# Performance work log

Hardware: AMD Instinct MI355X
Metric: run time of the kernel (lower is better)

The kernel has to match this reference:

```python
import math
import jax, jax.numpy as jnp
import numpy as np

D_MODEL = 1024
N_HEADS = 16
HEAD_DIM = D_MODEL // N_HEADS
ROPE_BASE = 10000.0
EPS = 1e-6


def rmsnorm(x, w, eps=EPS):
    # x: (..., head_dim); computed in fp32 like the torch code
    xf = x.astype(jnp.float32)
    rms = jax.lax.rsqrt(jnp.mean(xf * xf, axis=-1, keepdims=True) + eps)
    return (xf * rms).astype(x.dtype) * w


def apply_rope(x, cos, sin):
    # x: (B, H, T, head_dim); cos/sin: (T, head_dim/2)
    d2 = x.shape[-1] // 2
    x1, x2 = x[..., :d2], x[..., d2:]
    c = cos[None, None, :, :]
    s = sin[None, None, :, :]
    return jnp.concatenate([x1 * c - x2 * s, x2 * c + x1 * s], axis=-1)


def setup_inputs() -> dict:
    key = jax.random.key(0)
    ks = jax.random.split(key, 7)
    B, T = 2, 2048
    x = jax.random.normal(ks[0], (B, T, D_MODEL), dtype=jnp.float32)
    scale = 1.0 / math.sqrt(D_MODEL)
    Wq = jax.random.normal(ks[1], (D_MODEL, D_MODEL), dtype=jnp.float32) * scale
    Wk = jax.random.normal(ks[2], (D_MODEL, D_MODEL), dtype=jnp.float32) * scale
    Wv = jax.random.normal(ks[3], (D_MODEL, D_MODEL), dtype=jnp.float32) * scale
    Wo = jax.random.normal(ks[4], (D_MODEL, D_MODEL), dtype=jnp.float32) * scale
    q_norm_w = jnp.ones((HEAD_DIM,), dtype=jnp.float32)
    k_norm_w = jnp.ones((HEAD_DIM,), dtype=jnp.float32)
    return {"x": x, "Wq": Wq, "Wk": Wk, "Wv": Wv, "Wo": Wo,
            "q_norm_w": q_norm_w, "k_norm_w": k_norm_w}


def reference(x, Wq, Wk, Wv, Wo, q_norm_w, k_norm_w):
    B, T, d = x.shape
    H, hd = N_HEADS, HEAD_DIM
    # projections (nn.Linear applies x @ W.T; here W is stored as (in,out))
    q = (x @ Wq).reshape(B, T, H, hd).transpose(0, 2, 1, 3)  # (B,H,T,hd)
    k = (x @ Wk).reshape(B, T, H, hd).transpose(0, 2, 1, 3)
    v = (x @ Wv).reshape(B, T, H, hd).transpose(0, 2, 1, 3)
    # QK RMSNorm per head
    q = rmsnorm(q, q_norm_w)
    k = rmsnorm(k, k_norm_w)
    # rotary embeddings
    inv_freq = 1.0 / (ROPE_BASE ** (jnp.arange(0, hd, 2, dtype=jnp.float32) / hd))
    t = jnp.arange(T, dtype=jnp.float32)
    freqs = jnp.outer(t, inv_freq)  # (T, hd/2)
    cos, sin = jnp.cos(freqs), jnp.sin(freqs)
    q = apply_rope(q, cos, sin)
    k = apply_rope(k, cos, sin)
    # naive full attention with causal mask
    scale = 1.0 / math.sqrt(hd)
    attn = jnp.einsum('bhqd,bhkd->bhqk', q, k) * scale  # (B,H,T,T)
    causal = jnp.triu(jnp.full((T, T), -jnp.inf, dtype=attn.dtype), k=1)
    attn = attn + causal[None, None, :, :]
    attn = jax.nn.softmax(attn, axis=-1)
    out = jnp.einsum('bhqk,bhkd->bhqd', attn, v)
    out = out.transpose(0, 2, 1, 3).reshape(B, T, d)
    return out @ Wo
```

## Files before the change

### kernel.cpp

```cpp
#include <hip/hip_runtime.h>

typedef unsigned short u16;
typedef unsigned int   u32;
typedef __bf16 bf16x8 __attribute__((ext_vector_type(8)));
typedef float  f32x4  __attribute__((ext_vector_type(4)));
typedef float  f32x2  __attribute__((ext_vector_type(2)));
typedef u32    u32x4  __attribute__((ext_vector_type(4)));
typedef u16    u16x4  __attribute__((ext_vector_type(4)));

#define D_MODEL 1024
#define T_SEQ   2048
#define NH      16
#define HD      64

#define QSCALE  0.18033688011112042f
#define NEG8L2E -11.541560327111707f

__device__ __forceinline__ float b2f(u16 u){ return __uint_as_float(((u32)u)<<16); }
__device__ __forceinline__ u16 f2b(float f){
  u32 x = __float_as_uint(f);
  x += 0x7fffu + ((x>>16)&1u);
  return (u16)(x>>16);
}

__device__ __forceinline__ void gll16(const void* g, void* l){
  __builtin_amdgcn_global_load_lds((const __attribute__((address_space(1))) unsigned int*)g,
                                   (__attribute__((address_space(3))) unsigned int*)l, 16, 0, 0);
}

__global__ __launch_bounds__(256) void prep(
    const float* __restrict__ X, u16* __restrict__ Xb,
    const float* __restrict__ W0, const float* __restrict__ W1,
    const float* __restrict__ W2, const float* __restrict__ W3,
    u16* __restrict__ T0, u16* __restrict__ T1,
    u16* __restrict__ T2, u16* __restrict__ T3,
    float* __restrict__ cs)
{
  __shared__ u16 s[32][33];
  const int id = blockIdx.x, tid = threadIdx.x;
  if (id < 4096){
    const int i = (id*256 + tid)<<2;
    f32x4 v = *(const f32x4*)(X + i);
    u16x4 o;
    o[0]=f2b(v[0]); o[1]=f2b(v[1]); o[2]=f2b(v[2]); o[3]=f2b(v[3]);
    *(u16x4*)(Xb + i) = o;
  } else if (id < 8192){
    const int wid = id - 4096;
    const int z = wid >> 10, tile = wid & 1023;
    const float* src = (z==0)?W0:(z==1)?W1:(z==2)?W2:W3;
    u16*         dst = (z==0)?T0:(z==1)?T1:(z==2)?T2:T3;
    const int x = tid & 31, y = tid >> 5;
    const int r0 = (tile>>5)*32, c0 = (tile&31)*32;
    #pragma unroll
    for (int r=0;r<4;r++) s[y + r*8][x] = f2b(src[(r0 + y + r*8)*D_MODEL + c0 + x]);
    __syncthreads();
    #pragma unroll
    for (int r=0;r<4;r++) dst[(c0 + y + r*8)*D_MODEL + r0 + x] = s[x][y + r*8];
  } else {
    const int gid = (id-8192)*256 + tid;
    const int t = gid >> 5, fi = gid & 31;
    const float invf = expf(-(float)fi * 0.2878231366242558f);
    float sn, cn;
    sincosf((float)t * invf, &sn, &cn);
    cs[gid*2]   = cn;
    cs[gid*2+1] = sn;
  }
}

__global__ __launch_bounds__(256) void gemm_qkv(
    const u16* __restrict__ A, const u16* __restrict__ Bt,
    const float* __restrict__ qw, const float* __restrict__ kw,
    const float* __restrict__ cs,
    u16* __restrict__ Qb, u16* __restrict__ Kb, u16* __restrict__ Vt)
{
  __shared__ __align__(16) u16 sA[1024*8];
  __shared__ __align__(16) u16 sB[1024*8];
  const int id = blockIdx.x;
  const int xcd = id & 7, slot = id >> 3;
  const int bn = (xcd & 1)*12 + (slot % 12);
  const int bm = (xcd >> 1)*8 + (slot / 12);
  const int bm0 = bm<<7, bn0 = bn<<7;

  const int tid = threadIdx.x;
  const int lane = tid & 63;
  const int w  = tid>>6;
  const int wm = (w>>1)<<6;
  const int wn = (w&1)<<6;
  const int quad = lane>>4, lr = lane&15;
  const int swl = lr & 7;

  int rS[4], cS[4];
  #pragma unroll
  for (int i=0;i<4;i++){
    int s = i*256 + tid;
    rS[i] = s>>3;
    cS[i] = (s&7) ^ (rS[i]&7);
  }

  const f32x4 z4 = {0.f,0.f,0.f,0.f};
  f32x4 acc[4][4];
  #pragma unroll
  for (int i=0;i<4;i++)
    #pragma unroll
    for (int j=0;j<4;j++) acc[i][j] = z4;

  for (int kt=0; kt<D_MODEL; kt+=64){
    #pragma unroll
    for (int i=0;i<4;i++)
      gll16(A  + (bm0+rS[i])*D_MODEL + kt + cS[i]*8, sA + (i*256 + w*64)*8);
    #pragma unroll
    for (int i=0;i<4;i++)
      gll16(Bt + (bn0+rS[i])*D_MODEL + kt + cS[i]*8, sB + (i*256 + w*64)*8);
    __syncthreads();
    #pragma unroll
    for (int kk=0; kk<2; ++kk){
      bf16x8 af[4], bfr[4];
      const int cq = (kk*4 + quad) ^ swl;
      #pragma unroll
      for (int i=0;i<4;i++) af[i]  = *(const bf16x8*)(sA + ((wm + (i<<4) + lr)*8 + cq)*8);
      #pragma unroll
      for (int j=0;j<4;j++) bfr[j] = *(const bf16x8*)(sB + ((wn + (j<<4) + lr)*8 + cq)*8);
      #pragma unroll
      for (int i=0;i<4;i++)
        #pragma unroll
        for (int j=0;j<4;j++)
          acc[i][j] = __builtin_amdgcn_mfma_f32_16x16x32_bf16(af[i], bfr[j], acc[i][j], 0, 0, 0);
    }
    __syncthreads();
  }

  const int z = bn0 >> 10;
  const int ncl = bn0 & 1023;
  const int rq = quad<<2;

  if (z == 2){
    #pragma unroll
    for (int i=0;i<4;i++){
      int row0 = bm0 + wm + (i<<4) + rq;
      int bb = row0 >> 11, tt = row0 & (T_SEQ-1);
      #pragma unroll
      for (int j=0;j<4;j++){
        int nv = ncl + wn + (j<<4) + lr;
        int hh = nv >> 6, dd = nv & 63;
        u16* basep = Vt + ((bb*NH + hh)*HD + dd)*T_SEQ;
        #pragma unroll
        for (int r=0;r<4;r++){
          int t = tt + r;
          int pt = (t & ~63) + ((t&15)<<2) + ((t>>4)&3);
          basep[pt] = f2b(acc[i][j][r]);
        }
      }
    }
  } else {
    const float* w_ = (z==0) ? qw : kw;
    u16* dst = (z==0) ? Qb : Kb;
    const float scale = (z==0) ? QSCALE : 1.0f;
    float wv[4];
    #pragma unroll
    for (int j=0;j<4;j++) wv[j] = w_[(j<<4) + lr];
    #pragma unroll
    for (int i=0;i<4;i++){
      #pragma unroll
      for (int r=0;r<4;r++){
        const int grow = bm0 + wm + (i<<4) + rq + r;
        float ss = 0.f;
        #pragma unroll
        for (int j=0;j<4;j++) ss += acc[i][j][r]*acc[i][j][r];
        #pragma unroll
        for (int off=8; off>=1; off>>=1) ss += __shfl_xor(ss, off, 64);
        const float rms = rsqrtf(ss*(1.0f/64.0f) + 1e-6f);
        float xn[4];
        #pragma unroll
        for (int j=0;j<4;j++) xn[j] = acc[i][j][r]*rms*wv[j];
        const int t = grow & (T_SEQ-1);
        f32x2 c0 = *(const f32x2*)(cs + (t*32 + lr)*2);
        f32x2 c1 = *(const f32x2*)(cs + (t*32 + 16 + lr)*2);
        float o0 = xn[0]*c0[0] - xn[2]*c0[1];
        float o2 = xn[2]*c0[0] + xn[0]*c0[1];
        float o1 = xn[1]*c1[0] - xn[3]*c1[1];
        float o3 = xn[3]*c1[0] + xn[1]*c1[1];
        u16* rp = dst + grow*D_MODEL + ncl + wn + lr;
        rp[0]  = f2b(o0*scale);
        rp[16] = f2b(o1*scale);
        rp[32] = f2b(o2*scale);
        rp[48] = f2b(o3*scale);
      }
    }
  }
}

__global__ __launch_bounds__(256) void gemm_out(
    const u16* __restrict__ A, const u16* __restrict__ Bt, float* __restrict__ out)
{
  __shared__ __align__(16) u16 sA[512*8];
  __shared__ __align__(16) u16 sB[1024*8];
  const int id = blockIdx.x;
  const int xcd = id & 7, slot = id >> 3;
  const int bm = xcd*8 + (slot>>3);
  const int bn = slot & 7;
  const int bm0 = bm<<6, bn0 = bn<<7;

  const int tid = threadIdx.x;
  const int lane = tid & 63;
  const int w  = tid>>6;
  const int wm = (w>>1)<<5;
  const int wn = (w&1)<<6;
  const int quad = lane>>4, lr = lane&15;
  const int swl = lr & 7;

  int rS[4], cS[4];
  #pragma unroll
  for (int i=0;i<4;i++){
    int s = i*256 + tid;
    rS[i] = s>>3;
    cS[i] = (s&7) ^ (rS[i]&7);
  }

  const f32x4 z4 = {0.f,0.f,0.f,0.f};
  f32x4 acc[2][4];
  #pragma unroll
  for (int i=0;i<2;i++)
    #pragma unroll
    for (int j=0;j<4;j++) acc[i][j] = z4;

  for (int kt=0; kt<D_MODEL; kt+=64){
    #pragma unroll
    for (int i=0;i<2;i++)
      gll16(A  + (bm0+rS[i])*D_MODEL + kt + cS[i]*8, sA + (i*256 + w*64)*8);
    #pragma unroll
    for (int i=0;i<4;i++)
      gll16(Bt + (bn0+rS[i])*D_MODEL + kt + cS[i]*8, sB + (i*256 + w*64)*8);
    __syncthreads();
    #pragma unroll
    for (int kk=0; kk<2; ++kk){
      bf16x8 af[2], bfr[4];
      const int cq = (kk*4 + quad) ^ swl;
      #pragma unroll
      for (int i=0;i<2;i++) af[i]  = *(const bf16x8*)(sA + ((wm + (i<<4) + lr)*8 + cq)*8);
      #pragma unroll
      for (int j=0;j<4;j++) bfr[j] = *(const bf16x8*)(sB + ((wn + (j<<4) + lr)*8 + cq)*8);
      #pragma unroll
      for (int i=0;i<2;i++)
        #pragma unroll
        for (int j=0;j<4;j++)
          acc[i][j] = __builtin_amdgcn_mfma_f32_16x16x32_bf16(af[i], bfr[j], acc[i][j], 0, 0, 0);
    }
    __syncthreads();
  }

  const int rq = quad<<2;
  #pragma unroll
  for (int i=0;i<2;i++){
    #pragma unroll
    for (int r=0;r<4;r++){
      const int grow = bm0 + wm + (i<<4) + rq + r;
      #pragma unroll
      for (int j=0;j<4;j++)
        out[grow*D_MODEL + bn0 + wn + (j<<4) + lr] = acc[i][j][r];
    }
  }
}

__global__ __launch_bounds__(256) void attn_mfma(const u16* __restrict__ Qb, const u16* __restrict__ Kb,
                                                 const u16* __restrict__ Vt, u16* __restrict__ AO)
{
  __shared__ __align__(16) u16 sK [2][4096];
  __shared__ __align__(16) u16 sVT[2][4096];
  __shared__ __align__(16) u16 sP [4][1024];
  const int tid = threadIdx.x;
  const int h  = blockIdx.x, b = blockIdx.y;
  const int qt = 31 - blockIdx.z;
  const int w = tid>>6, lane = tid&63;
  const int quad = lane>>4, lr = lane&15;
  const int q8 = quad<<3;

  const int s0 = w*64 + lane, s1 = 256 + w*64 + lane;
  const int r0s = s0>>3, c0s = (s0&7)^(r0s&7);
  const int r1s = s1>>3, c1s = (s1&7)^(r1s&7);
  const u16* Kbase = Kb + (b*T_SEQ)*D_MODEL + h*HD;
  const u16* Vbase = Vt + (b*NH + h)*HD*T_SEQ;
  const int ldsOff0 = (w*64)*8, ldsOff1 = (256 + w*64)*8;

  const u16* Qrow = Qb + (b*T_SEQ + qt*64 + w*16 + lr)*D_MODEL + h*HD;
  bf16x8 qf0 = *(const bf16x8*)(Qrow + q8);
  bf16x8 qf1 = *(const bf16x8*)(Qrow + 32 + q8);

  f32x4 o[4];
  float lp[4];
  const f32x4 z4 = {0.f,0.f,0.f,0.f};
  const f32x4 ci = {NEG8L2E, NEG8L2E, NEG8L2E, NEG8L2E};
  #pragma unroll
  for (int r=0;r<4;r++) lp[r] = 0.f;
  #pragma unroll
  for (int nt=0;nt<4;nt++) o[nt] = z4;

  u16* myP = sP[w];

  gll16(Kbase + r0s*D_MODEL + c0s*8, &sK[0][ldsOff0]);
  gll16(Kbase + r1s*D_MODEL + c1s*8, &sK[0][ldsOff1]);
  gll16(Vbase + r0s*T_SEQ + c0s*8,   &sVT[0][ldsOff0]);
  gll16(Vbase + r1s*T_SEQ + c1s*8,   &sVT[0][ldsOff1]);
  __syncthreads();

  for (int kt=0; kt<=qt; ++kt){
    const int cur = kt&1;
    if (kt < qt){
      const int kn = kt+1, nb = cur^1;
      gll16(Kbase + (kn*64 + r0s)*D_MODEL + c0s*8, &sK[nb][ldsOff0]);
      gll16(Kbase + (kn*64 + r1s)*D_MODEL + c1s*8, &sK[nb][ldsOff1]);
      gll16(Vbase + r0s*T_SEQ + kn*64 + c0s*8,     &sVT[nb][ldsOff0]);
      gll16(Vbase + r1s*T_SEQ + kn*64 + c1s*8,     &sVT[nb][ldsOff1]);
    }

    f32x4 s4[4];
    #pragma unroll
    for (int ct=0; ct<4; ++ct){
      const int row = ct*16 + lr;
      const int sw = row&7;
      bf16x8 k0 = *(const bf16x8*)(&sK[cur][(row*8 + (quad     ^ sw))*8]);
      bf16x8 k1 = *(const bf16x8*)(&sK[cur][(row*8 + ((4+quad) ^ sw))*8]);
      f32x4 acc = ci;
      acc = __builtin_amdgcn_mfma_f32_16x16x32_bf16(qf0, k0, acc, 0,0,0);
      acc = __builtin_amdgcn_mfma_f32_16x16x32_bf16(qf1, k1, acc, 0,0,0);
      s4[ct] = acc;
    }

    if (kt == qt){
      #pragma unroll
      for (int ct=0; ct<4; ++ct){
        int col = ct*16 + lr;
        #pragma unroll
        for (int r=0;r<4;r++)
          if (col > w*16 + quad*4 + r) s4[ct][r] = -1e30f;
      }
    }

    #pragma unroll
    for (int r=0;r<4;r++){
      u16x4 pk;
      #pragma unroll
      for (int ct=0; ct<4; ++ct){
        float p = exp2f(s4[ct][r]);
        u32 pu = __float_as_uint(p) & 0xffff0000u;
        lp[r] += __uint_as_float(pu);
        pk[ct] = (u16)(pu>>16);
      }
      const int prow = quad*4 + r;
      const int pidx = prow*64 + (((lr>>1) ^ (prow&7))<<3) + ((lr&1)<<2);
      *(u16x4*)(myP + pidx) = pk;
    }

    #pragma unroll
    for (int st=0; st<2; ++st){
      bf16x8 pf = *(const bf16x8*)(myP + lr*64 + (((st*4+quad) ^ (lr&7))<<3));
      #pragma unroll
      for (int nt=0;nt<4;nt++){
        const int row = nt*16 + lr;
        const int slotv = row*8 + ((st*4+quad) ^ (row&7));
        bf16x8 vf = *(const bf16x8*)(&sVT[cur][slotv*8]);
        o[nt] = __builtin_amdgcn_mfma_f32_16x16x32_bf16(pf, vf, o[nt], 0,0,0);
      }
    }
    __syncthreads();
  }

  #pragma unroll
  for (int r=0;r<4;r++){
    #pragma unroll
    for (int off=8; off>=1; off>>=1) lp[r] += __shfl_xor(lp[r], off, 64);
  }
  const int rowg = b*T_SEQ + qt*64 + w*16 + quad*4;
  #pragma unroll
  for (int r=0;r<4;r++){
    float inv = 1.0f / lp[r];
    #pragma unroll
    for (int nt=0;nt<4;nt++)
      AO[(rowg + r)*D_MODEL + h*HD + nt*16 + lr] = f2b(o[nt][r]*inv);
  }
}

extern "C" void kernel_launch(void* const* d_in, const int* in_sizes, int n_in,
                              void* d_out, int out_size, void* d_ws, size_t ws_size,
                              hipStream_t stream)
{
  const float* X  = (const float*)d_in[0];
  const float* Wq = (const float*)d_in[1];
  const float* Wk = (const float*)d_in[2];
  const float* Wv = (const float*)d_in[3];
  const float* Wo = (const float*)d_in[4];
  const float* qw = (const float*)d_in[5];
  const float* kw = (const float*)d_in[6];

  char* ws = (char*)d_ws;
  const size_t MB = 1024*1024;
  u16*   WqkvT = (u16*)(ws + 0*MB);
  u16*   WoT   = (u16*)(ws + 6*MB);
  u16*   Xb    = (u16*)(ws + 8*MB);
  u16*   Qb    = (u16*)(ws + 16*MB);
  u16*   Kb    = (u16*)(ws + 24*MB);
  u16*   Vt    = (u16*)(ws + 32*MB);
  u16*   AO    = (u16*)(ws + 40*MB);
  float* CS    = (float*)(ws + 48*MB);

  prep<<<dim3(8448), 256, 0, stream>>>(X, Xb, Wq, Wk, Wv, Wo,
      WqkvT, WqkvT + 1024*1024, WqkvT + 2*1024*1024, WoT, CS);
  gemm_qkv<<<dim3(768), 256, 0, stream>>>(Xb, WqkvT, qw, kw, CS, Qb, Kb, Vt);
  attn_mfma<<<dim3(NH, 2, 32), 256, 0, stream>>>(Qb, Kb, Vt, AO);
  gemm_out<<<dim3(512), 256, 0, stream>>>(AO, WoT, (float*)d_out);
}
```

Before: 185.9 us.

## Vectorize weight transpose, halve gemm_out M-tile, single-buffer V in attention

The weight transpose in prep now reads float4 and writes u16x4 per thread instead of scalar accesses, to cut memory instructions. gemm_out switches to 32-row tiles with twice as many blocks, aiming for better occupancy and CU coverage at the cost of more B-tile reloads. The attention kernel drops V double buffering: it loads V into one LDS buffer at the start of each iteration and adds a barrier before the PV matmul. This saves LDS but puts the V load latency on the critical path, and the extra barrier adds synchronization cost.

```diff
diff --git a/kernel.cpp b/kernel.cpp
--- a/kernel.cpp
+++ b/kernel.cpp
@@ -49,13 +49,16 @@
     const int z = wid >> 10, tile = wid & 1023;
     const float* src = (z==0)?W0:(z==1)?W1:(z==2)?W2:W3;
     u16*         dst = (z==0)?T0:(z==1)?T1:(z==2)?T2:T3;
-    const int x = tid & 31, y = tid >> 5;
+    const int x = tid & 7, y = tid >> 3;
     const int r0 = (tile>>5)*32, c0 = (tile&31)*32;
-    #pragma unroll
-    for (int r=0;r<4;r++) s[y + r*8][x] = f2b(src[(r0 + y + r*8)*D_MODEL + c0 + x]);
-    __syncthreads();
-    #pragma unroll
-    for (int r=0;r<4;r++) dst[(c0 + y + r*8)*D_MODEL + r0 + x] = s[x][y + r*8];
+    f32x4 v = *(const f32x4*)(src + (r0 + y)*D_MODEL + c0 + 4*x);
+    #pragma unroll
+    for (int k=0;k<4;k++) s[y][4*x+k] = f2b(v[k]);
+    __syncthreads();
+    u16x4 o;
+    #pragma unroll
+    for (int k=0;k<4;k++) o[k] = s[4*x+k][y];
+    *(u16x4*)(dst + (c0 + y)*D_MODEL + r0 + 4*x) = o;
   } else {
     const int gid = (id-8192)*256 + tid;
     const int t = gid >> 5, fi = gid & 31;
@@ -192,72 +195,62 @@
 __global__ __launch_bounds__(256) void gemm_out(
     const u16* __restrict__ A, const u16* __restrict__ Bt, float* __restrict__ out)
 {
-  __shared__ __align__(16) u16 sA[512*8];
+  __shared__ __align__(16) u16 sA[256*8];
   __shared__ __align__(16) u16 sB[1024*8];
   const int id = blockIdx.x;
   const int xcd = id & 7, slot = id >> 3;
-  const int bm = xcd*8 + (slot>>3);
+  const int bm = xcd*16 + (slot>>3);
   const int bn = slot & 7;
-  const int bm0 = bm<<6, bn0 = bn<<7;
+  const int bm0 = bm<<5, bn0 = bn<<7;
 
   const int tid = threadIdx.x;
   const int lane = tid & 63;
   const int w  = tid>>6;
-  const int wm = (w>>1)<<5;
+  const int wm = (w>>1)<<4;
   const int wn = (w&1)<<6;
   const int quad = lane>>4, lr = lane&15;
   const int swl = lr & 7;
 
-  int rS[4], cS[4];
+  const int rA = tid>>3, cA = (tid&7) ^ (rA&7);
+  int rB[4], cB[4];
   #pragma unroll
   for (int i=0;i<4;i++){
     int s = i*256 + tid;
-    rS[i] = s>>3;
-    cS[i] = (s&7) ^ (rS[i]&7);
+    rB[i] = s>>3;
+    cB[i] = (s&7) ^ (rB[i]&7);
   }
 
   const f32x4 z4 = {0.f,0.f,0.f,0.f};
-  f32x4 acc[2][4];
-  #pragma unroll
-  for (int i=0;i<2;i++)
-    #pragma unroll
-    for (int j=0;j<4;j++) acc[i][j] = z4;
+  f32x4 acc[4];
+  #pragma unroll
+  for (int j=0;j<4;j++) acc[j] = z4;
 
   for (int kt=0; kt<D_MODEL; kt+=64){
-    #pragma unroll
-    for (int i=0;i<2;i++)
-      gll16(A  + (bm0+rS[i])*D_MODEL + kt + cS[i]*8, sA + (i*256 + w*64)*8);
+    gll16(A + (bm0+rA)*D_MODEL + kt + cA*8, sA + (w*64)*8);
     #pragma unroll
     for (int i=0;i<4;i++)
-      gll16(Bt + (bn0+rS[i])*D_MODEL + kt + cS[i]*8, sB + (i*256 + w*64)*8);
+      gll16(Bt + (bn0+rB[i])*D_MODEL + kt + cB[i]*8, sB + (i*256 + w*64)*8);
     __syncthreads();
     #pragma unroll
     for (int kk=0; kk<2; ++kk){
-      bf16x8 af[2], bfr[4];
       const int cq = (kk*4 + quad) ^ swl;
-      #pragma unroll
-      for (int i=0;i<2;i++) af[i]  = *(const bf16x8*)(sA + ((wm + (i<<4) + lr)*8 + cq)*8);
-      #pragma unroll
-      for (int j=0;j<4;j++) bfr[j] = *(const bf16x8*)(sB + ((wn + (j<<4) + lr)*8 + cq)*8);
-      #pragma unroll
-      for (int i=0;i<2;i++)
-        #pragma unroll
-        for (int j=0;j<4;j++)
-          acc[i][j] = __builtin_amdgcn_mfma_f32_16x16x32_bf16(af[i], bfr[j], acc[i][j], 0, 0, 0);
+      bf16x8 af = *(const bf16x8*)(sA + ((wm + lr)*8 + cq)*8);
+      #pragma unroll
+      for (int j=0;j<4;j++){
+        bf16x8 bfr = *(const bf16x8*)(sB + ((wn + (j<<4) + lr)*8 + cq)*8);
+        acc[j] = __builtin_amdgcn_mfma_f32_16x16x32_bf16(af, bfr, acc[j], 0, 0, 0);
+      }
     }
     __syncthreads();
   }
 
   const int rq = quad<<2;
   #pragma unroll
-  for (int i=0;i<2;i++){
-    #pragma unroll
-    for (int r=0;r<4;r++){
-      const int grow = bm0 + wm + (i<<4) + rq + r;
-      #pragma unroll
-      for (int j=0;j<4;j++)
-        out[grow*D_MODEL + bn0 + wn + (j<<4) + lr] = acc[i][j][r];
-    }
+  for (int r=0;r<4;r++){
+    const int grow = bm0 + wm + rq + r;
+    #pragma unroll
+    for (int j=0;j<4;j++)
+      out[grow*D_MODEL + bn0 + wn + (j<<4) + lr] = acc[j][r];
   }
 }
 
@@ -265,7 +258,7 @@
                                                  const u16* __restrict__ Vt, u16* __restrict__ AO)
 {
   __shared__ __align__(16) u16 sK [2][4096];
-  __shared__ __align__(16) u16 sVT[2][4096];
+  __shared__ __align__(16) u16 sV [4096];
   __shared__ __align__(16) u16 sP [4][1024];
   const int tid = threadIdx.x;
   const int h  = blockIdx.x, b = blockIdx.y;
@@ -298,8 +291,6 @@
 
   gll16(Kbase + r0s*D_MODEL + c0s*8, &sK[0][ldsOff0]);
   gll16(Kbase + r1s*D_MODEL + c1s*8, &sK[0][ldsOff1]);
-  gll16(Vbase + r0s*T_SEQ + c0s*8,   &sVT[0][ldsOff0]);
-  gll16(Vbase + r1s*T_SEQ + c1s*8,   &sVT[0][ldsOff1]);
   __syncthreads();
 
   for (int kt=0; kt<=qt; ++kt){
@@ -308,9 +299,9 @@
       const int kn = kt+1, nb = cur^1;
       gll16(Kbase + (kn*64 + r0s)*D_MODEL + c0s*8, &sK[nb][ldsOff0]);
       gll16(Kbase + (kn*64 + r1s)*D_MODEL + c1s*8, &sK[nb][ldsOff1]);
-      gll16(Vbase + r0s*T_SEQ + kn*64 + c0s*8,     &sVT[nb][ldsOff0]);
-      gll16(Vbase + r1s*T_SEQ + kn*64 + c1s*8,     &sVT[nb][ldsOff1]);
-    }
+    }
+    gll16(Vbase + r0s*T_SEQ + kt*64 + c0s*8, &sV[ldsOff0]);
+    gll16(Vbase + r1s*T_SEQ + kt*64 + c1s*8, &sV[ldsOff1]);
 
     f32x4 s4[4];
     #pragma unroll
@@ -350,6 +341,8 @@
       *(u16x4*)(myP + pidx) = pk;
     }
 
+    __syncthreads();
+
     #pragma unroll
     for (int st=0; st<2; ++st){
       bf16x8 pf = *(const bf16x8*)(myP + lr*64 + (((st*4+quad) ^ (lr&7))<<3));
@@ -357,7 +350,7 @@
       for (int nt=0;nt<4;nt++){
         const int row = nt*16 + lr;
         const int slotv = row*8 + ((st*4+quad) ^ (row&7));
-        bf16x8 vf = *(const bf16x8*)(&sVT[cur][slotv*8]);
+        bf16x8 vf = *(const bf16x8*)(&sV[slotv*8]);
         o[nt] = __builtin_amdgcn_mfma_f32_16x16x32_bf16(pf, vf, o[nt], 0,0,0);
       }
     }
@@ -406,5 +399,5 @@
       WqkvT, WqkvT + 1024*1024, WqkvT + 2*1024*1024, WoT, CS);
   gemm_qkv<<<dim3(768), 256, 0, stream>>>(Xb, WqkvT, qw, kw, CS, Qb, Kb, Vt);
   attn_mfma<<<dim3(NH, 2, 32), 256, 0, stream>>>(Qb, Kb, Vt, AO);
-  gemm_out<<<dim3(512), 256, 0, stream>>>(AO, WoT, (float*)d_out);
-}
+  gemm_out<<<dim3(1024), 256, 0, stream>>>(AO, WoT, (float*)d_out);
+}
```

After: 191.8 us. +3.2%, slower.
